# Optimization experiments

Measured on AMD Instinct MI355X. Metric: run time of the kernel, lower is better.

## Reference

```python
import jax, jax.numpy as jnp
import numpy as np

N, IN_DIM, HEADS, OUT_DIM, EDGE_DIM = 3072, 128, 4, 64, 8
EPS = 1e-5


def setup_inputs() -> dict:
    key = jax.random.key(0)
    ks = jax.random.split(key, 8)
    x = jax.random.normal(ks[0], (N, IN_DIM), dtype=jnp.float32)
    adj = jax.random.randint(ks[1], (N, N), 0, 2, dtype=jnp.int32)
    edge_feats = jax.random.normal(ks[2], (N, N, EDGE_DIM), dtype=jnp.float32)
    W = jax.random.normal(ks[3], (IN_DIM, HEADS * OUT_DIM), dtype=jnp.float32) * (IN_DIM ** -0.5)
    a_src = jax.random.normal(ks[4], (HEADS, OUT_DIM), dtype=jnp.float32) * 0.01
    a_dst = jax.random.normal(ks[5], (HEADS, OUT_DIM), dtype=jnp.float32) * 0.01
    ep_w = jax.random.normal(ks[6], (EDGE_DIM, HEADS), dtype=jnp.float32) * (EDGE_DIM ** -0.5)
    ep_b = jax.random.normal(ks[7], (HEADS,), dtype=jnp.float32) * 0.01
    gamma = jnp.ones((HEADS * OUT_DIM,), dtype=jnp.float32)
    beta = jnp.zeros((HEADS * OUT_DIM,), dtype=jnp.float32)
    return {"x": x, "adj": adj, "edge_feats": edge_feats, "W": W, "a_src": a_src,
            "a_dst": a_dst, "ep_w": ep_w, "ep_b": ep_b, "gamma": gamma, "beta": beta}


def reference(x, adj, edge_feats, W, a_src, a_dst, ep_w, ep_b, gamma, beta):
    n = x.shape[0]
    h = (x @ W).reshape(n, HEADS, OUT_DIM)                      # (N,H,D)
    s_src = jnp.einsum('nhd,hd->nh', h, a_src)                  # (N,H)
    s_dst = jnp.einsum('nhd,hd->nh', h, a_dst)                  # (N,H)
    edge_attn = jnp.einsum('ije,eh->ijh', edge_feats, ep_w) + ep_b  # (N,N,H)
    attn = s_src[:, None, :] + s_dst[None, :, :] + edge_attn    # (N,N,H)
    attn = jax.nn.leaky_relu(attn, 0.2)
    neg = jnp.finfo(attn.dtype).min
    attn = jnp.where((adj == 0)[:, :, None], neg, attn)
    attn = jax.nn.softmax(attn, axis=1)                         # softmax over neighbors j
    # dropout is identity in eval mode
    out = jnp.einsum('ijh,jhd->ihd', attn, h).reshape(n, HEADS * OUT_DIM)
    mean = out.mean(-1, keepdims=True)
    var = out.var(-1, keepdims=True)
    out = (out - mean) * jax.lax.rsqrt(var + EPS) * gamma + beta
    return out
```

## Files before the change

kernel.cpp:

```cpp
#include <hip/hip_runtime.h>

#define NN     3072
#define INDIM  128
#define NH     4
#define DD     64
#define CC     256
#define EE     8
#define NODE_T 8
#define TI16   16
#define BJ     64
#define JSPLIT 8
#define JRANGE (NN / JSPLIT)
#define NTS    (JRANGE / BJ)
#define PTJ    72
#define NCH    (NN / 32)

typedef short short8v __attribute__((ext_vector_type(8)));
typedef unsigned short ushort8v __attribute__((ext_vector_type(8)));
typedef float float4v __attribute__((ext_vector_type(4)));

__device__ __forceinline__ float bf2f(unsigned short u) {
    return __uint_as_float(((unsigned int)u) << 16);
}
__device__ __forceinline__ unsigned short f2bf(float f) {
    unsigned int u = __float_as_uint(f);
    u += 0x7fffu + ((u >> 16) & 1u);
    return (unsigned short)(u >> 16);
}
__device__ __forceinline__ float rfl(float f) {
    return __int_as_float(__builtin_amdgcn_readfirstlane(__float_as_int(f)));
}

__global__ __launch_bounds__(256) void hproj(
    const float* __restrict__ x,
    const float* __restrict__ W,
    const float* __restrict__ a_src,
    const float* __restrict__ a_dst,
    unsigned short* __restrict__ htf,
    float* __restrict__ s_src,
    float* __restrict__ s_dst)
{
    const int tid = threadIdx.x;
    const int n0  = blockIdx.x * NODE_T;
    const int h   = tid >> 6, lane = tid & 63;

    float acc[NODE_T] = {};
#pragma unroll 4
    for (int k = 0; k < INDIM; ++k) {
        const float wv = W[(size_t)k * CC + tid];
#pragma unroll
        for (int n = 0; n < NODE_T; ++n)
            acc[n] = fmaf(x[(size_t)(n0 + n) * INDIM + k], wv, acc[n]);
    }

    ushort8v hv;
#pragma unroll
    for (int n = 0; n < NODE_T; ++n) hv[n] = f2bf(acc[n]);
    unsigned short* dst = htf
        + (size_t)((h * 4 + (lane >> 4)) * NCH + (n0 >> 5)) * 512
        + (size_t)((((n0 >> 3) & 3) * 16 + (lane & 15)) * 8);
    *reinterpret_cast<ushort8v*>(dst) = hv;

    const float asv = a_src[h * DD + lane];
    const float adv = a_dst[h * DD + lane];
#pragma unroll
    for (int n = 0; n < NODE_T; ++n) {
        float s1 = acc[n] * asv, s2 = acc[n] * adv;
#pragma unroll
        for (int off = 32; off > 0; off >>= 1) {
            s1 += __shfl_xor(s1, off, 64);
            s2 += __shfl_xor(s2, off, 64);
        }
        if (lane == 0) {
            s_src[(size_t)(n0 + n) * NH + h] = s1;
            s_dst[(size_t)(n0 + n) * NH + h] = s2;
        }
    }
}

__global__ __launch_bounds__(256) void gat_fused(
    const int* __restrict__ adj,
    const float* __restrict__ ef,
    const unsigned short* __restrict__ htf,
    const float* __restrict__ s_src,
    const float* __restrict__ s_dst,
    const float* __restrict__ ep_w,
    const float* __restrict__ ep_b,
    float* __restrict__ out_part,
    float* __restrict__ l_part)
{
    __shared__ unsigned short pt[2][NH][16][PTJ];

    const int tid  = threadIdx.x;
    const int rw   = tid >> 6;
    const int lane = tid & 63;
    const int l15  = lane & 15;
    const int q    = lane >> 4;
    const int bid  = blockIdx.x;
    const int s    = bid & (JSPLIT - 1);
    const int i0   = (bid >> 3) * TI16;
    const int jb0  = s * JRANGE;

    float epw[EE][NH];
#pragma unroll
    for (int e = 0; e < EE; ++e)
#pragma unroll
        for (int h = 0; h < NH; ++h) epw[e][h] = rfl(ep_w[e * NH + h]);
    float sb[4][NH];
#pragma unroll
    for (int r = 0; r < 4; ++r)
#pragma unroll
        for (int h = 0; h < NH; ++h)
            sb[r][h] = rfl(s_src[(size_t)(i0 + rw * 4 + r) * NH + h] + ep_b[h]);

    float4v acc[4];
#pragma unroll
    for (int f = 0; f < 4; ++f) acc[f] = (float4v){0.f, 0.f, 0.f, 0.f};
    float l_loc[4][4] = {};

    float4 efA[4], efB[4], sd4;
    int    ajr[4];

#define LOADP(JN) do {                                                       \
        const int jj = (JN) + lane;                                          \
        sd4 = *reinterpret_cast<const float4*>(s_dst + (size_t)jj * NH);     \
        _Pragma("unroll")                                                    \
        for (int r = 0; r < 4; ++r) {                                        \
            const size_t ro = (size_t)(i0 + rw * 4 + r) * NN;                \
            ajr[r] = adj[ro + jj];                                           \
            const float* ep = ef + (ro + jj) * EE;                           \
            efA[r] = *reinterpret_cast<const float4*>(ep);                   \
            efB[r] = *reinterpret_cast<const float4*>(ep + 4);               \
        } } while (0)

#define SCOREP(NB) do {                                                      \
        const float sdh[4] = {sd4.x, sd4.y, sd4.z, sd4.w};                   \
        _Pragma("unroll")                                                    \
        for (int r = 0; r < 4; ++r) {                                        \
            const float ev[EE] = {efA[r].x, efA[r].y, efA[r].z, efA[r].w,    \
                                  efB[r].x, efB[r].y, efB[r].z, efB[r].w};   \
            _Pragma("unroll")                                                \
            for (int h = 0; h < NH; ++h) {                                   \
                float sc = sb[r][h] + sdh[h];                                \
                _Pragma("unroll")                                            \
                for (int e = 0; e < EE; ++e)                                 \
                    sc = fmaf(ev[e], epw[e][h], sc);                         \
                sc = (sc > 0.f) ? sc : 0.2f * sc;                            \
                const float p = (ajr[r] == 0) ? 0.f : __expf(sc);            \
                const unsigned short bb = f2bf(p);                           \
                l_loc[r][h] += bf2f(bb);                                     \
                pt[NB][h][rw * 4 + r][lane] = bb;                            \
            } } } while (0)

    LOADP(jb0);
    SCOREP(0);
    __syncthreads();

    int buf = 0;
    for (int t = 0; t < NTS; ++t) {
        const int cid0 = (jb0 + t * BJ) >> 5;
        const bool pf  = (t + 1 < NTS);

        short8v bfrag[2][4];
#pragma unroll
        for (int ks = 0; ks < 2; ++ks)
#pragma unroll
            for (int f = 0; f < 4; ++f)
                bfrag[ks][f] = *reinterpret_cast<const short8v*>(
                    htf + (size_t)((rw * 4 + f) * NCH + cid0 + ks) * 512 + lane * 8);
        __builtin_amdgcn_sched_barrier(0);

        if (pf) LOADP(jb0 + (t + 1) * BJ);
        __builtin_amdgcn_sched_barrier(0);

#pragma unroll
        for (int ks = 0; ks < 2; ++ks) {
            const short8v a = *reinterpret_cast<const short8v*>(
                &pt[buf][rw][l15][ks * 32 + q * 8]);
#pragma unroll
            for (int f = 0; f < 4; ++f)
                acc[f] = __builtin_amdgcn_mfma_f32_16x16x32_bf16(a, bfrag[ks][f], acc[f], 0, 0, 0);
        }

        if (pf) SCOREP(buf ^ 1);
        __syncthreads();
        buf ^= 1;
    }
#undef LOADP
#undef SCOREP

#pragma unroll
    for (int r = 0; r < 4; ++r)
#pragma unroll
        for (int h = 0; h < NH; ++h) {
            float v = l_loc[r][h];
#pragma unroll
            for (int off = 32; off > 0; off >>= 1) v += __shfl_xor(v, off, 64);
            if (lane == 0)
                l_part[((size_t)s * NN + i0 + rw * 4 + r) * NH + h] = v;
        }

#pragma unroll
    for (int f = 0; f < 4; ++f)
#pragma unroll
        for (int rg = 0; rg < 4; ++rg)
            out_part[((size_t)s * NN + i0 + q * 4 + rg) * CC + rw * DD + f * 16 + l15] = acc[f][rg];
}

__global__ __launch_bounds__(256) void gat_ln(
    const float* __restrict__ out_part,
    const float* __restrict__ l_part,
    const float* __restrict__ gamma,
    const float* __restrict__ beta,
    float* __restrict__ out)
{
    const int tid = threadIdx.x, w = tid >> 6, lane = tid & 63;
    const int i = blockIdx.x * 4 + w;

    float v[4];
#pragma unroll
    for (int k = 0; k < 4; ++k) {
        float a = 0.f;
#pragma unroll
        for (int sp = 0; sp < JSPLIT; ++sp)
            a += out_part[((size_t)sp * NN + i) * CC + k * 64 + lane];
        float lb = 0.f;
#pragma unroll
        for (int sp = 0; sp < JSPLIT; ++sp)
            lb += l_part[((size_t)sp * NN + i) * NH + k];
        v[k] = a / lb;
    }

    float s1 = v[0] + v[1] + v[2] + v[3];
    float s2 = v[0] * v[0] + v[1] * v[1] + v[2] * v[2] + v[3] * v[3];
#pragma unroll
    for (int off = 32; off > 0; off >>= 1) {
        s1 += __shfl_xor(s1, off, 64);
        s2 += __shfl_xor(s2, off, 64);
    }
    const float mean = s1 * (1.f / CC);
    const float var  = s2 * (1.f / CC) - mean * mean;
    const float rstd = rsqrtf(var + 1e-5f);
    float* op = out + (size_t)i * CC;
#pragma unroll
    for (int k = 0; k < 4; ++k) {
        const int c = k * 64 + lane;
        op[c] = (v[k] - mean) * rstd * gamma[c] + beta[c];
    }
}

extern "C" void kernel_launch(void* const* d_in, const int* in_sizes, int n_in,
                              void* d_out, int out_size, void* d_ws, size_t ws_size,
                              hipStream_t stream) {
    const float* x     = (const float*)d_in[0];
    const int*   adj   = (const int*)d_in[1];
    const float* ef    = (const float*)d_in[2];
    const float* W     = (const float*)d_in[3];
    const float* a_src = (const float*)d_in[4];
    const float* a_dst = (const float*)d_in[5];
    const float* ep_w  = (const float*)d_in[6];
    const float* ep_b  = (const float*)d_in[7];
    const float* gamma = (const float*)d_in[8];
    const float* beta  = (const float*)d_in[9];

    float* s_src = (float*)d_ws;
    float* s_dst = s_src + (size_t)NN * NH;
    unsigned short* htf = (unsigned short*)(s_dst + (size_t)NN * NH);
    float* out_part = (float*)(htf + (size_t)NN * CC);
    float* l_part   = out_part + (size_t)JSPLIT * NN * CC;
    (void)ws_size; (void)in_sizes; (void)n_in; (void)out_size;

    hipLaunchKernelGGL(hproj, dim3(NN / NODE_T), dim3(256), 0, stream,
                       x, W, a_src, a_dst, htf, s_src, s_dst);
    hipLaunchKernelGGL(gat_fused, dim3((NN / TI16) * JSPLIT), dim3(256), 0, stream,
                       adj, ef, htf, s_src, s_dst, ep_w, ep_b, out_part, l_part);
    hipLaunchKernelGGL(gat_ln, dim3(NN / 4), dim3(256), 0, stream,
                       out_part, l_part, gamma, beta, (float*)d_out);
}
```

Before: 476.8 us.

## Split fused attention into score kernel writing bf16 P and MFMA PV kernel

Unfuses the score computation from the PV matmul. A row-per-wave gat_score kernel streams adj and edge features once and writes unnormalized bf16 probabilities to a global buffer laid out in MFMA fragment order, along with the full row sums. A separate gat_pv kernel then does the bf16 MFMA product over 4 K-splits. This drops the LDS double buffering and syncs and simplifies the LN reduction, at the cost of writing and re-reading an extra N*N*H bf16 buffer (about 75 MB) through global memory.

```diff
diff --git a/kernel.cpp b/kernel.cpp
--- a/kernel.cpp
+++ b/kernel.cpp
@@ -7,13 +7,10 @@
 #define CC     256
 #define EE     8
 #define NODE_T 8
-#define TI16   16
-#define BJ     64
-#define JSPLIT 8
-#define JRANGE (NN / JSPLIT)
-#define NTS    (JRANGE / BJ)
-#define PTJ    72
-#define NCH    (NN / 32)
+#define NJC    (NN / 32)
+#define CHSZ   (NH * 16 * 32)
+#define KSPLIT 4
+#define NCPS   (NJC / KSPLIT)
 
 typedef short short8v __attribute__((ext_vector_type(8)));
 typedef unsigned short ushort8v __attribute__((ext_vector_type(8)));
@@ -57,7 +54,7 @@
 #pragma unroll
     for (int n = 0; n < NODE_T; ++n) hv[n] = f2bf(acc[n]);
     unsigned short* dst = htf
-        + (size_t)((h * 4 + (lane >> 4)) * NCH + (n0 >> 5)) * 512
+        + (size_t)((h * 4 + (lane >> 4)) * NJC + (n0 >> 5)) * 512
         + (size_t)((((n0 >> 3) & 3) * 16 + (lane & 15)) * 8);
     *reinterpret_cast<ushort8v*>(dst) = hv;
 
@@ -78,127 +75,116 @@
     }
 }
 
-__global__ __launch_bounds__(256) void gat_fused(
+__global__ __launch_bounds__(256) void gat_score(
     const int* __restrict__ adj,
     const float* __restrict__ ef,
-    const unsigned short* __restrict__ htf,
     const float* __restrict__ s_src,
     const float* __restrict__ s_dst,
     const float* __restrict__ ep_w,
     const float* __restrict__ ep_b,
-    float* __restrict__ out_part,
-    float* __restrict__ l_part)
-{
-    __shared__ unsigned short pt[2][NH][16][PTJ];
-
+    unsigned short* __restrict__ Pf,
+    float* __restrict__ lsum)
+{
+    const int tid  = threadIdx.x;
+    const int w    = tid >> 6;
+    const int lane = tid & 63;
+    const int i    = blockIdx.x * 4 + w;
+
+    float epw[EE][NH];
+#pragma unroll
+    for (int e = 0; e < EE; ++e)
+#pragma unroll
+        for (int h = 0; h < NH; ++h) epw[e][h] = rfl(ep_w[e * NH + h]);
+    float sb[NH];
+#pragma unroll
+    for (int h = 0; h < NH; ++h)
+        sb[h] = rfl(s_src[(size_t)i * NH + h] + ep_b[h]);
+
+    const size_t ro = (size_t)i * NN;
+    const size_t prow = (size_t)(i >> 4) * NJC * CHSZ + (size_t)(i & 15) * 32;
+
+    float l_loc[NH] = {0.f, 0.f, 0.f, 0.f};
+
+    for (int jb = 0; jb < NN; jb += 128) {
+        const int j0 = jb + 2 * lane;
+        const int2   a2  = *reinterpret_cast<const int2*>(adj + ro + j0);
+        const float* ep  = ef + (ro + j0) * EE;
+        const float4 e0  = *reinterpret_cast<const float4*>(ep);
+        const float4 e1  = *reinterpret_cast<const float4*>(ep + 4);
+        const float4 e2  = *reinterpret_cast<const float4*>(ep + 8);
+        const float4 e3  = *reinterpret_cast<const float4*>(ep + 12);
+        const float4 sda = *reinterpret_cast<const float4*>(s_dst + (size_t)j0 * NH);
+        const float4 sdb = *reinterpret_cast<const float4*>(s_dst + (size_t)j0 * NH + 4);
+
+        const float eva[EE]  = {e0.x, e0.y, e0.z, e0.w, e1.x, e1.y, e1.z, e1.w};
+        const float evb[EE]  = {e2.x, e2.y, e2.z, e2.w, e3.x, e3.y, e3.z, e3.w};
+        const float sdha[NH] = {sda.x, sda.y, sda.z, sda.w};
+        const float sdhb[NH] = {sdb.x, sdb.y, sdb.z, sdb.w};
+
+        unsigned int* pw = reinterpret_cast<unsigned int*>(
+            Pf + prow + (size_t)(j0 >> 5) * CHSZ + (j0 & 31));
+
+#pragma unroll
+        for (int h = 0; h < NH; ++h) {
+            float sa = sb[h] + sdha[h];
+            float sc = sb[h] + sdhb[h];
+#pragma unroll
+            for (int e = 0; e < EE; ++e) {
+                sa = fmaf(eva[e], epw[e][h], sa);
+                sc = fmaf(evb[e], epw[e][h], sc);
+            }
+            sa = (sa > 0.f) ? sa : 0.2f * sa;
+            sc = (sc > 0.f) ? sc : 0.2f * sc;
+            const float pa = (a2.x == 0) ? 0.f : __expf(sa);
+            const float pb = (a2.y == 0) ? 0.f : __expf(sc);
+            const unsigned int ba = f2bf(pa), bb = f2bf(pb);
+            l_loc[h] += bf2f((unsigned short)ba) + bf2f((unsigned short)bb);
+            pw[h * 256] = ba | (bb << 16);
+        }
+    }
+
+#pragma unroll
+    for (int h = 0; h < NH; ++h) {
+        float v = l_loc[h];
+#pragma unroll
+        for (int off = 32; off > 0; off >>= 1) v += __shfl_xor(v, off, 64);
+        if (lane == 0) lsum[(size_t)i * NH + h] = v;
+    }
+}
+
+__global__ __launch_bounds__(256) void gat_pv(
+    const unsigned short* __restrict__ Pf,
+    const unsigned short* __restrict__ htf,
+    float* __restrict__ out_part)
+{
     const int tid  = threadIdx.x;
     const int rw   = tid >> 6;
     const int lane = tid & 63;
     const int l15  = lane & 15;
     const int q    = lane >> 4;
     const int bid  = blockIdx.x;
-    const int s    = bid & (JSPLIT - 1);
-    const int i0   = (bid >> 3) * TI16;
-    const int jb0  = s * JRANGE;
-
-    float epw[EE][NH];
-#pragma unroll
-    for (int e = 0; e < EE; ++e)
-#pragma unroll
-        for (int h = 0; h < NH; ++h) epw[e][h] = rfl(ep_w[e * NH + h]);
-    float sb[4][NH];
-#pragma unroll
-    for (int r = 0; r < 4; ++r)
-#pragma unroll
-        for (int h = 0; h < NH; ++h)
-            sb[r][h] = rfl(s_src[(size_t)(i0 + rw * 4 + r) * NH + h] + ep_b[h]);
+    const int s    = bid & (KSPLIT - 1);
+    const int it   = bid >> 2;
+    const int i0   = it * 16;
 
     float4v acc[4];
 #pragma unroll
     for (int f = 0; f < 4; ++f) acc[f] = (float4v){0.f, 0.f, 0.f, 0.f};
-    float l_loc[4][4] = {};
-
-    float4 efA[4], efB[4], sd4;
-    int    ajr[4];
-
-#define LOADP(JN) do {                                                       \
-        const int jj = (JN) + lane;                                          \
-        sd4 = *reinterpret_cast<const float4*>(s_dst + (size_t)jj * NH);     \
-        _Pragma("unroll")                                                    \
-        for (int r = 0; r < 4; ++r) {                                        \
-            const size_t ro = (size_t)(i0 + rw * 4 + r) * NN;                \
-            ajr[r] = adj[ro + jj];                                           \
-            const float* ep = ef + (ro + jj) * EE;                           \
-            efA[r] = *reinterpret_cast<const float4*>(ep);                   \
-            efB[r] = *reinterpret_cast<const float4*>(ep + 4);               \
-        } } while (0)
-
-#define SCOREP(NB) do {                                                      \
-        const float sdh[4] = {sd4.x, sd4.y, sd4.z, sd4.w};                   \
-        _Pragma("unroll")                                                    \
-        for (int r = 0; r < 4; ++r) {                                        \
-            const float ev[EE] = {efA[r].x, efA[r].y, efA[r].z, efA[r].w,    \
-                                  efB[r].x, efB[r].y, efB[r].z, efB[r].w};   \
-            _Pragma("unroll")                                                \
-            for (int h = 0; h < NH; ++h) {                                   \
-                float sc = sb[r][h] + sdh[h];                                \
-                _Pragma("unroll")                                            \
-                for (int e = 0; e < EE; ++e)                                 \
-                    sc = fmaf(ev[e], epw[e][h], sc);                         \
-                sc = (sc > 0.f) ? sc : 0.2f * sc;                            \
-                const float p = (ajr[r] == 0) ? 0.f : __expf(sc);            \
-                const unsigned short bb = f2bf(p);                           \
-                l_loc[r][h] += bf2f(bb);                                     \
-                pt[NB][h][rw * 4 + r][lane] = bb;                            \
-            } } } while (0)
-
-    LOADP(jb0);
-    SCOREP(0);
-    __syncthreads();
-
-    int buf = 0;
-    for (int t = 0; t < NTS; ++t) {
-        const int cid0 = (jb0 + t * BJ) >> 5;
-        const bool pf  = (t + 1 < NTS);
-
-        short8v bfrag[2][4];
-#pragma unroll
-        for (int ks = 0; ks < 2; ++ks)
-#pragma unroll
-            for (int f = 0; f < 4; ++f)
-                bfrag[ks][f] = *reinterpret_cast<const short8v*>(
-                    htf + (size_t)((rw * 4 + f) * NCH + cid0 + ks) * 512 + lane * 8);
-        __builtin_amdgcn_sched_barrier(0);
-
-        if (pf) LOADP(jb0 + (t + 1) * BJ);
-        __builtin_amdgcn_sched_barrier(0);
-
-#pragma unroll
-        for (int ks = 0; ks < 2; ++ks) {
-            const short8v a = *reinterpret_cast<const short8v*>(
-                &pt[buf][rw][l15][ks * 32 + q * 8]);
-#pragma unroll
-            for (int f = 0; f < 4; ++f)
-                acc[f] = __builtin_amdgcn_mfma_f32_16x16x32_bf16(a, bfrag[ks][f], acc[f], 0, 0, 0);
-        }
-
-        if (pf) SCOREP(buf ^ 1);
-        __syncthreads();
-        buf ^= 1;
-    }
-#undef LOADP
-#undef SCOREP
-
-#pragma unroll
-    for (int r = 0; r < 4; ++r)
-#pragma unroll
-        for (int h = 0; h < NH; ++h) {
-            float v = l_loc[r][h];
-#pragma unroll
-            for (int off = 32; off > 0; off >>= 1) v += __shfl_xor(v, off, 64);
-            if (lane == 0)
-                l_part[((size_t)s * NN + i0 + rw * 4 + r) * NH + h] = v;
-        }
+
+    const unsigned short* Abase = Pf + (size_t)it * NJC * CHSZ
+                                + (size_t)rw * 512 + (size_t)l15 * 32 + q * 8;
+    const unsigned short* Bbase = htf + (size_t)lane * 8;
+
+    for (int cc = 0; cc < NCPS; ++cc) {
+        const int ch = s * NCPS + cc;
+        const short8v a = *reinterpret_cast<const short8v*>(Abase + (size_t)ch * CHSZ);
+#pragma unroll
+        for (int f = 0; f < 4; ++f) {
+            const short8v b = *reinterpret_cast<const short8v*>(
+                Bbase + (size_t)((rw * 4 + f) * NJC + ch) * 512);
+            acc[f] = __builtin_amdgcn_mfma_f32_16x16x32_bf16(a, b, acc[f], 0, 0, 0);
+        }
+    }
 
 #pragma unroll
     for (int f = 0; f < 4; ++f)
@@ -209,7 +195,7 @@
 
 __global__ __launch_bounds__(256) void gat_ln(
     const float* __restrict__ out_part,
-    const float* __restrict__ l_part,
+    const float* __restrict__ lsum,
     const float* __restrict__ gamma,
     const float* __restrict__ beta,
     float* __restrict__ out)
@@ -222,13 +208,9 @@
     for (int k = 0; k < 4; ++k) {
         float a = 0.f;
 #pragma unroll
-        for (int sp = 0; sp < JSPLIT; ++sp)
+        for (int sp = 0; sp < KSPLIT; ++sp)
             a += out_part[((size_t)sp * NN + i) * CC + k * 64 + lane];
-        float lb = 0.f;
-#pragma unroll
-        for (int sp = 0; sp < JSPLIT; ++sp)
-            lb += l_part[((size_t)sp * NN + i) * NH + k];
-        v[k] = a / lb;
+        v[k] = a / lsum[(size_t)i * NH + k];
     }
 
     float s1 = v[0] + v[1] + v[2] + v[3];
@@ -265,15 +247,18 @@
 
     float* s_src = (float*)d_ws;
     float* s_dst = s_src + (size_t)NN * NH;
-    unsigned short* htf = (unsigned short*)(s_dst + (size_t)NN * NH);
-    float* out_part = (float*)(htf + (size_t)NN * CC);
-    float* l_part   = out_part + (size_t)JSPLIT * NN * CC;
+    float* lsum  = s_dst + (size_t)NN * NH;
+    unsigned short* htf = (unsigned short*)(lsum + (size_t)NN * NH);
+    unsigned short* Pf  = htf + (size_t)NN * CC;
+    float* out_part = (float*)(Pf + (size_t)NN * NN * NH);
     (void)ws_size; (void)in_sizes; (void)n_in; (void)out_size;
 
     hipLaunchKernelGGL(hproj, dim3(NN / NODE_T), dim3(256), 0, stream,
                        x, W, a_src, a_dst, htf, s_src, s_dst);
-    hipLaunchKernelGGL(gat_fused, dim3((NN / TI16) * JSPLIT), dim3(256), 0, stream,
-                       adj, ef, htf, s_src, s_dst, ep_w, ep_b, out_part, l_part);
+    hipLaunchKernelGGL(gat_score, dim3(NN / 4), dim3(256), 0, stream,
+                       adj, ef, s_src, s_dst, ep_w, ep_b, Pf, lsum);
+    hipLaunchKernelGGL(gat_pv, dim3((NN / 16) * KSPLIT), dim3(256), 0, stream,
+                       Pf, htf, out_part);
     hipLaunchKernelGGL(gat_ln, dim3(NN / 4), dim3(256), 0, stream,
-                       out_part, l_part, gamma, beta, (float*)d_out);
-}
+                       out_part, lsum, gamma, beta, (float*)d_out);
+}
```

Result: slower. 505.7 us (+6.1%).
